# Performance work log

Measured on AMD Instinct MI355X. Metric: run time of the kernel, lower is better.

The kernel has to match this reference:

```python
import jax, jax.numpy as jnp
import numpy as np

B, S, D_TEXT, MAXF = 2, 1024, 384, 5
D_MODEL, N_HEADS, D_FF, L = 768, 12, 3072, 4
HEAD_DIM = D_MODEL // N_HEADS
EPS = 1e-6
NEG = -1e9


def _rms(x, g):
    return x * jax.lax.rsqrt(jnp.mean(x * x, axis=-1, keepdims=True) + EPS) * g


def _attn(x, w, mask):
    # w: [4, d, d] = (wq, wk, wv, wo); mask: [b, s, s] bool (True = attend)
    b, s, d = x.shape

    def proj(W):
        return jnp.einsum('bsd,de->bse', x, W).reshape(b, s, N_HEADS, HEAD_DIM).transpose(0, 2, 1, 3)

    q, k, v = proj(w[0]), proj(w[1]), proj(w[2])
    scale = jnp.asarray(1.0 / np.sqrt(HEAD_DIM), x.dtype)
    scores = jnp.einsum('bhqe,bhke->bhqk', q, k) * scale
    scores = jnp.where(mask[:, None], scores, NEG)
    p = jax.nn.softmax(scores, axis=-1)
    o = jnp.einsum('bhqk,bhke->bhqe', p, v).transpose(0, 2, 1, 3).reshape(b, s, d)
    return jnp.einsum('bsd,de->bse', o, w[3])


def _forward(number_values, datetime_values, boolean_values, text_values, column_name_values,
             W_cn, b_cn, W_num, b_num, W_text, b_text, W_dt, b_dt, W_bool, b_bool,
             g_cn, g_num, g_text, g_dt, g_bool, mask_emb,
             blk_norms, blk_attn, blk_up, blk_gate, blk_down,
             g_out, Wd_num, bd_num, Wd_dt, bd_dt, Wd_bool, bd_bool, Wd_text, bd_text,
             node_indices, table_name_indices, column_name_indices,
             f2p_neighbor_indices, semantic_types, masks, is_padding):
    valid = ~is_padding
    pv = valid[:, :, None] & valid[:, None, :]  # [b,s,s]
    eye = jnp.eye(S, dtype=bool)[None]
    same_node = node_indices[:, :, None] == node_indices[:, None, :]
    col_mask = ((column_name_indices[:, :, None] == column_name_indices[:, None, :])
                & (table_name_indices[:, :, None] == table_name_indices[:, None, :]) & pv) | eye
    feat_mask = (same_node & pv) | eye
    # kv node is one of q's f2p neighbors
    nei = (f2p_neighbor_indices[:, :, :, None] == node_indices[:, None, None, :]).any(axis=2)
    nei_mask = ((nei | same_node) & pv) | eye
    full_mask = pv | eye

    # per-semantic-type value encoders (Linear + RMSNorm)
    cn = _rms(column_name_values @ W_cn + b_cn, g_cn)
    num_e = _rms(number_values @ W_num + b_num, g_num)
    text_e = _rms(text_values @ W_text + b_text, g_text)
    dt_e = _rms(datetime_values @ W_dt + b_dt, g_dt)
    bool_e = _rms(boolean_values @ W_bool + b_bool, g_bool)
    st = semantic_types[..., None]
    val = jnp.where(st == 0, num_e, jnp.where(st == 1, text_e, jnp.where(st == 2, dt_e, bool_e)))
    # masked cells get the learned mask embedding for their semantic type
    val = jnp.where(masks[..., None], mask_emb[semantic_types], val)
    x = val + cn

    for i in range(L):
        nw, aw = blk_norms[i], blk_attn[i]
        x = x + _attn(_rms(x, nw[0]), aw[0], col_mask)
        x = x + _attn(_rms(x, nw[1]), aw[1], feat_mask)
        x = x + _attn(_rms(x, nw[2]), aw[2], nei_mask)
        x = x + _attn(_rms(x, nw[3]), aw[3], full_mask)
        h = _rms(x, nw[4])
        x = x + (jax.nn.silu(h @ blk_gate[i]) * (h @ blk_up[i])) @ blk_down[i]

    h = _rms(x, g_out)
    return (h @ Wd_num + bd_num, h @ Wd_dt + bd_dt, h @ Wd_bool + bd_bool, h @ Wd_text + bd_text)


def setup_inputs() -> dict:
    key = jax.random.key(0)
    ks = iter(jax.random.split(key, 64))

    def nrm(shape, scale=0.02):
        return jax.random.normal(next(ks), shape, jnp.float32) * scale

    inp = {}
    inp['number_values'] = jax.random.normal(next(ks), (B, S, 1), jnp.float32)
    inp['datetime_values'] = jax.random.normal(next(ks), (B, S, 1), jnp.float32)
    inp['boolean_values'] = jax.random.normal(next(ks), (B, S, 1), jnp.float32)
    inp['text_values'] = jax.random.normal(next(ks), (B, S, D_TEXT), jnp.float32)
    inp['column_name_values'] = jax.random.normal(next(ks), (B, S, D_TEXT), jnp.float32)
    inp['W_cn'] = nrm((D_TEXT, D_MODEL)); inp['b_cn'] = jnp.zeros((D_MODEL,), jnp.float32)
    inp['W_num'] = nrm((1, D_MODEL)); inp['b_num'] = jnp.zeros((D_MODEL,), jnp.float32)
    inp['W_text'] = nrm((D_TEXT, D_MODEL)); inp['b_text'] = jnp.zeros((D_MODEL,), jnp.float32)
    inp['W_dt'] = nrm((1, D_MODEL)); inp['b_dt'] = jnp.zeros((D_MODEL,), jnp.float32)
    inp['W_bool'] = nrm((1, D_MODEL)); inp['b_bool'] = jnp.zeros((D_MODEL,), jnp.float32)
    for n in ('g_cn', 'g_num', 'g_text', 'g_dt', 'g_bool'):
        inp[n] = jnp.ones((D_MODEL,), jnp.float32)
    inp['mask_emb'] = jax.random.normal(next(ks), (4, D_MODEL), jnp.float32)
    inp['blk_norms'] = jnp.ones((L, 5, D_MODEL), jnp.float32)
    inp['blk_attn'] = nrm((L, 4, 4, D_MODEL, D_MODEL))
    inp['blk_up'] = nrm((L, D_MODEL, D_FF))
    inp['blk_gate'] = nrm((L, D_MODEL, D_FF))
    inp['blk_down'] = nrm((L, D_FF, D_MODEL))
    inp['g_out'] = jnp.ones((D_MODEL,), jnp.float32)
    inp['Wd_num'] = nrm((D_MODEL, 1)); inp['bd_num'] = jnp.zeros((1,), jnp.float32)
    inp['Wd_dt'] = nrm((D_MODEL, 1)); inp['bd_dt'] = jnp.zeros((1,), jnp.float32)
    inp['Wd_bool'] = nrm((D_MODEL, 1)); inp['bd_bool'] = jnp.zeros((1,), jnp.float32)
    inp['Wd_text'] = nrm((D_MODEL, D_TEXT)); inp['bd_text'] = jnp.zeros((D_TEXT,), jnp.float32)
    inp['node_indices'] = jax.random.randint(next(ks), (B, S), 0, 128)
    inp['table_name_indices'] = jax.random.randint(next(ks), (B, S), 0, 8)
    inp['column_name_indices'] = jax.random.randint(next(ks), (B, S), 0, 32)
    inp['f2p_neighbor_indices'] = jax.random.randint(next(ks), (B, S, MAXF), 0, 128)
    inp['semantic_types'] = jax.random.randint(next(ks), (B, S), 0, 4)
    inp['masks'] = jax.random.bernoulli(next(ks), 0.15, (B, S))
    inp['is_padding'] = jnp.zeros((B, S), bool)
    return inp


def reference(number_values, datetime_values, boolean_values, text_values, column_name_values,
              W_cn, b_cn, W_num, b_num, W_text, b_text, W_dt, b_dt, W_bool, b_bool,
              g_cn, g_num, g_text, g_dt, g_bool, mask_emb,
              blk_norms, blk_attn, blk_up, blk_gate, blk_down,
              g_out, Wd_num, bd_num, Wd_dt, bd_dt, Wd_bool, bd_bool, Wd_text, bd_text,
              node_indices, table_name_indices, column_name_indices,
              f2p_neighbor_indices, semantic_types, masks, is_padding):
    return _forward(number_values, datetime_values, boolean_values, text_values, column_name_values,
                    W_cn, b_cn, W_num, b_num, W_text, b_text, W_dt, b_dt, W_bool, b_bool,
                    g_cn, g_num, g_text, g_dt, g_bool, mask_emb,
                    blk_norms, blk_attn, blk_up, blk_gate, blk_down,
                    g_out, Wd_num, bd_num, Wd_dt, bd_dt, Wd_bool, bd_bool, Wd_text, bd_text,
                    node_indices, table_name_indices, column_name_indices,
                    f2p_neighbor_indices, semantic_types, masks, is_padding)
```

## Files before the change

### kernel.cpp

```cpp
#include <hip/hip_runtime.h>
#include <hip/hip_bf16.h>
#include <cmath>
#include <stdint.h>


#define BB 2
#define SS 1024
#define DT 384
#define DM 768
#define NH 12
#define DH 64
#define DFF 3072
#define NL 4
#define NROW (BB*SS)
#define EPSF 1e-6f
#define QSC 0.1803368801111244f

typedef unsigned short u16;
typedef unsigned char u8;
typedef unsigned int u32;
typedef __attribute__((ext_vector_type(8))) short s16x8;
typedef __attribute__((ext_vector_type(4))) float f32x4;

__device__ __forceinline__ u16 f2bu(float f){
    u32 x = __float_as_uint(f);
    u32 r = (x + 0x7fffu + ((x>>16)&1u)) >> 16;
    return (u16)r;
}
__device__ __forceinline__ u32 pk2(float lo, float hi){
    return (u32)f2bu(lo) | ((u32)f2bu(hi)<<16);
}
__device__ __forceinline__ int swz(int row, int c){
    return (row<<6) + (((((c>>3) ^ row) & 7))<<3) + (c&7);
}
__device__ __forceinline__ float rsum16(float v){
    v += __shfl_xor(v,1); v += __shfl_xor(v,2);
    v += __shfl_xor(v,4); v += __shfl_xor(v,8);
    return v;
}
#define SBAR() __builtin_amdgcn_sched_barrier(0)
#define GLDS(src,dst) __builtin_amdgcn_global_load_lds((const __attribute__((address_space(1))) u32*)(src), (__attribute__((address_space(3))) u32*)(dst), 16, 0, 0)
#define GLDS4(src,dst) __builtin_amdgcn_global_load_lds((const __attribute__((address_space(1))) u32*)(src), (__attribute__((address_space(3))) u32*)(dst), 4, 0, 0)

__global__ void zero_f(float* __restrict__ p, int n){
    int i = blockIdx.x*256 + threadIdx.x;
    if (i<n) p[i]=0.f;
}

__device__ void norm_bool_body(const void* __restrict__ src, u8* __restrict__ dst, int n)
{
    __shared__ int fl[4];
    if (threadIdx.x<4) fl[threadIdx.x]=0;
    __syncthreads();
    const u32* wsrc = (const u32*)src;
    const int nw = n/4;
    int any=0, nb=0, hi=0, lo=0;
    for (int i=threadIdx.x;i<nw;i+=blockDim.x){
        u32 v=wsrc[i];
        if (!v) continue;
        any=1;
        #pragma unroll
        for (int b=0;b<4;b++){
            u32 by=(v>>(8*b))&0xffu;
            if (by>1u) nb=1;
            if (by==1u && b!=0) hi=1;
        }
        if ((v&0xffffu)==0x3f80u) lo=1;
    }
    if (any) atomicOr(&fl[0],1);
    if (nb)  atomicOr(&fl[1],1);
    if (hi)  atomicOr(&fl[2],1);
    if (lo)  atomicOr(&fl[3],1);
    __syncthreads();
    int c;
    if (!fl[0]) c=0;
    else if (!fl[1]) c = fl[2] ? 2 : 1;
    else if (fl[3]) c = 3;
    else c = 1;
    for (int i=threadIdx.x;i<n;i+=blockDim.x){
        u8 v;
        if (c==0)      v=0;
        else if (c==1) v = (((const u32*)src)[i]!=0u);
        else if (c==2) v = (((const u8*)src)[i]!=0u);
        else           v = (((const u16*)src)[i]!=0u);
        dst[i]=v;
    }
}
__global__ void norm_bool2(const void* s0, u8* d0, const void* s1, u8* d1, int n)
{
    if (blockIdx.x==0) norm_bool_body(s0,d0,n);
    else               norm_bool_body(s1,d1,n);
}

__global__ void pack_meta(const int* __restrict__ node, const int* __restrict__ colx,
                          const int* __restrict__ tbl, const u8* __restrict__ pad,
                          u32* __restrict__ pm, int n)
{
    int i = blockIdx.x*256 + threadIdx.x;
    if (i<n)
        pm[i] = (u32)(node[i]&0xff) | ((u32)(colx[i]&0xff)<<8) | ((u32)(tbl[i]&0xff)<<16) | ((u32)(pad[i]&1)<<24);
}

__global__ __launch_bounds__(256) void mask4_kernel(const u32* __restrict__ pm, const int* __restrict__ f2p,
                                                    u8* __restrict__ m4)
{
    const int b = blockIdx.y, kg = blockIdx.x;
    const int t = threadIdx.x;
    __shared__ u32 qm[1024];
    __shared__ int qf[1024*5];
    for (int i=t;i<1024;i+=256) qm[i] = pm[b*SS+i];
    for (int i=t;i<5*1024;i+=256) qf[i] = f2p[b*SS*5 + i];
    __syncthreads();
    const int q0 = t*4;
    u32 qmv[4]; int qn[4]; int qfv[4][5];
    #pragma unroll
    for (int j=0;j<4;j++){
        qmv[j]=qm[q0+j]; qn[j]=(int)(qmv[j]&0xffu);
        #pragma unroll
        for (int f=0;f<5;f++) qfv[j][f]=qf[(q0+j)*5+f];
    }
    for (int kk=0;kk<16;kk++){
        const int k = kg*16+kk;
        const u32 km = qm[k];
        const int kn = (int)(km&0xffu);
        u32 outw=0;
        #pragma unroll
        for (int j=0;j<4;j++){
            const u32 qmw = qmv[j];
            const bool pv = (((qmw|km)>>24)&1u)==0u;
            u32 by=0;
            if ((((qmw^km)&0x00ffff00u)==0u) && pv) by|=1;
            if ((((qmw^km)&0xffu)==0u) && pv) by|=2;
            bool nei = (qfv[j][0]==kn)||(qfv[j][1]==kn)||(qfv[j][2]==kn)||(qfv[j][3]==kn)||(qfv[j][4]==kn)
                       ||(qn[j]==kn);
            if (nei && pv) by|=4;
            if (pv) by|=8;
            if ((q0+j)==k) by=15;
            outw |= by<<(8*j);
        }
        ((u32*)(m4 + ((size_t)b<<20) + ((size_t)k<<10)))[t] = outw;
    }
}

__global__ __launch_bounds__(256) void transpose_cvt2(const float* __restrict__ src, u16* __restrict__ dst,
                                                      int K, int N, size_t dz,
                                                      const float* __restrict__ gbase, int gmode)
{
    const int z = blockIdx.z;
    src += (size_t)z*K*N;
    dst += (size_t)z*dz;
    const float* g = nullptr;
    if (gmode==1){ int m = z&3; if (m<3) g = gbase + (size_t)((z>>4)*5 + ((z>>2)&3))*768; }
    else if (gmode==2){ g = gbase + (size_t)z*5*768; }
    const int n0 = blockIdx.x*32, k0 = blockIdx.y*64;
    __shared__ float t[64][33];
    const int tid = threadIdx.x;
    const int kr = tid>>3, n4 = (tid&7)*4;
    #pragma unroll
    for (int p=0;p<2;p++){
        const int k = p*32 + kr;
        float gk = g ? g[k0+k] : 1.f;
        float4 v = *(const float4*)(src + (size_t)(k0+k)*N + n0 + n4);
        t[k][n4]=v.x*gk; t[k][n4+1]=v.y*gk; t[k][n4+2]=v.z*gk; t[k][n4+3]=v.w*gk;
    }
    __syncthreads();
    const int n = tid>>3, ks = (tid&7)*8;
    const int ng = n0 + n;
    uint4 o;
    u32* op = (u32*)&o;
    #pragma unroll
    for (int i=0;i<4;i++)
        op[i] = pk2(t[ks+2*i][n], t[ks+2*i+1][n]);
    *(uint4*)&dst[(((size_t)(ng>>7)*(K>>6) + (k0>>6))<<13) + ((ng&127)<<6) + ks] = o;
}

__global__ __launch_bounds__(256) void cvt_tiled2(const float* __restrict__ s0, u16* __restrict__ d0,
                                                  const float* __restrict__ s1, u16* __restrict__ d1, int K)
{
    const float* src = blockIdx.y ? s1 : s0;
    u16* dst = blockIdx.y ? d1 : d0;
    const int gid = blockIdx.x*256 + threadIdx.x;
    const int base = gid*8;
    const int row = base / K, col = base - row*K;
    float4 a = *(const float4*)(src + base);
    float4 b = *(const float4*)(src + base + 4);
    uint4 o;
    o.x = pk2(a.x,a.y); o.y = pk2(a.z,a.w);
    o.z = pk2(b.x,b.y); o.w = pk2(b.z,b.w);
    *(uint4*)&dst[(((size_t)(row>>7)*(K>>6) + (col>>6))<<13) + ((row&127)<<6) + (col&63)] = o;
}

__device__ __forceinline__ void stage3(const u16* aT, const u16* bT, int cb, int brow,
                                       u16* la, u16* lb, int w, int l)
{
    #pragma unroll
    for (int p=0;p<2;p++){
        const int q = p*256 + w*64 + l;
        const int row = q>>2, u = q&3;
        const int so = row*64 + cb + (((u ^ ((row>>1)&3))&3)<<3);
        GLDS(aT+so, la + p*2048 + w*512);
    }
    {
        const int q = w*64 + l;
        const int row = q>>2, u = q&3;
        const int so = (brow+row)*64 + cb + (((u ^ ((row>>1)&3))&3)<<3);
        GLDS(bT+so, lb + w*512);
    }
}

__global__ __launch_bounds__(256,4) void gemm_t(
    const u16* __restrict__ At, const u16* __restrict__ Bt,
    int K, int AMS, u16* __restrict__ qk16, u16* __restrict__ vt16,
    const float* __restrict__ rs_in)
{
    __shared__ u16 lds[3][6144];
    const int tid = threadIdx.x;
    const int lane = tid & 63, w = tid >> 6;
    const int cg = lane >> 4, cl = lane & 15;
    const int NT = K >> 5;
    const int n0 = blockIdx.x*64;
    const int brow = n0 & 64;
    const size_t bNb = (size_t)(n0>>7)*(K>>6);

    const u16* aB = At + ((size_t)blockIdx.y * AMS << 13);
    const u16* bB = Bt + (bNb << 13);

    f32x4 acc[2][4];
    #pragma unroll
    for (int i=0;i<2;i++)
        #pragma unroll
        for (int j=0;j<4;j++) acc[i][j] = (f32x4){0.f,0.f,0.f,0.f};

    stage3(aB, bB, 0,  brow, &lds[0][0], &lds[0][4096], w, lane);
    stage3(aB, bB, 32, brow, &lds[1][0], &lds[1][4096], w, lane);

    for (int kt=0; kt<NT; kt++){
        const int buf = kt % 3;
        if (kt+2 < NT){
            const int k2 = kt+2;
            stage3(aB + ((size_t)(k2>>1)<<13), bB + ((size_t)(k2>>1)<<13),
                   (k2&1)<<5, brow, &lds[k2%3][0], &lds[k2%3][4096], w, lane);
            asm volatile("s_waitcnt vmcnt(6)" ::: "memory");
        } else if (kt+1 < NT){
            asm volatile("s_waitcnt vmcnt(3)" ::: "memory");
        } else {
            asm volatile("s_waitcnt vmcnt(0)" ::: "memory");
        }
        SBAR(); __builtin_amdgcn_s_barrier(); SBAR();
        s16x8 af[2], bf[4];
        #pragma unroll
        for (int mt=0;mt<2;mt++){
            const int ra = w*32 + mt*16 + cl;
            af[mt] = *(const s16x8*)&lds[buf][ra*32 + (((cg ^ ((ra>>1)&3))&3)<<3)];
        }
        #pragma unroll
        for (int nt=0;nt<4;nt++){
            const int rb = nt*16 + cl;
            bf[nt] = *(const s16x8*)&lds[buf][4096 + rb*32 + (((cg ^ ((rb>>1)&3))&3)<<3)];
        }
        #pragma unroll
        for (int mt=0;mt<2;mt++)
            #pragma unroll
            for (int nt=0;nt<4;nt++)
                acc[mt][nt] = __builtin_amdgcn_mfma_f32_16x16x32_bf16(af[mt], bf[nt], acc[mt][nt], 0,0,0);
        SBAR(); __builtin_amdgcn_s_barrier(); SBAR();
    }

    const int m0 = blockIdx.y*128;
    #pragma unroll
    for (int mt=0;mt<2;mt++){
        const int grow0 = m0 + w*32 + mt*16 + cg*4;
        float rr[4];
        #pragma unroll
        for (int j=0;j<4;j++) rr[j] = rsqrtf(rs_in[grow0+j]*(1.f/768.f) + EPSF);
        #pragma unroll
        for (int nt=0;nt<4;nt++){
            const int col = n0 + nt*16 + cl;
            if (col < 768){
                #pragma unroll
                for (int j=0;j<4;j++)
                    qk16[(size_t)(grow0+j)*1536 + col] = f2bu(acc[mt][nt][j]*rr[j]*QSC);
            } else if (col < 1536){
                #pragma unroll
                for (int j=0;j<4;j++)
                    qk16[(size_t)(grow0+j)*1536 + col] = f2bu(acc[mt][nt][j]*rr[j]);
            } else {
                const int b = grow0>>10, s0 = grow0&1023;
                const int dhg = col - 1536;
                uint2 o;
                o.x = pk2(acc[mt][nt][0]*rr[0], acc[mt][nt][1]*rr[1]);
                o.y = pk2(acc[mt][nt][2]*rr[2], acc[mt][nt][3]*rr[3]);
                *(uint2*)(vt16 + ((size_t)(b*768 + dhg)<<10) + s0) = o;
            }
        }
    }
}

__global__ __launch_bounds__(256,3) void gemm_gu(
    const u16* __restrict__ At, const u16* __restrict__ Bg, const u16* __restrict__ Bu,
    const float* __restrict__ rs_in, u16* __restrict__ o16)
{
    __shared__ u16 lds[3][8192];
    const int tid = threadIdx.x;
    const int lane = tid & 63, w = tid >> 6;
    const int cg = lane >> 4, cl = lane & 15;
    const int NT = 24;
    const int n0 = blockIdx.x*64;
    const int brow = n0 & 64;
    const size_t bNb = (size_t)(n0>>7)*12;

    const u16* aB = At + ((size_t)blockIdx.y * 12 << 13);
    const u16* gB = Bg + (bNb << 13);
    const u16* uB = Bu + (bNb << 13);

    f32x4 accg[2][4], accu[2][4];
    #pragma unroll
    for (int i=0;i<2;i++)
        #pragma unroll
        for (int j=0;j<4;j++){ accg[i][j] = (f32x4){0.f,0.f,0.f,0.f}; accu[i][j] = (f32x4){0.f,0.f,0.f,0.f}; }

    #define STAGE_GU(kt2, cb, buf) { \
        const u16* a_ = aB + ((size_t)(kt2)<<13); \
        const u16* g_ = gB + ((size_t)(kt2)<<13); \
        const u16* u_ = uB + ((size_t)(kt2)<<13); \
        _Pragma("unroll") \
        for (int p=0;p<2;p++){ \
            const int q = p*256 + w*64 + lane; \
            const int row = q>>2, uu = q&3; \
            const int so = row*64 + (cb) + (((uu ^ ((row>>1)&3))&3)<<3); \
            GLDS(a_+so, &lds[buf][0] + p*2048 + w*512); \
        } \
        { \
            const int q = w*64 + lane; \
            const int row = q>>2, uu = q&3; \
            const int so = (brow+row)*64 + (cb) + (((uu ^ ((row>>1)&3))&3)<<3); \
            GLDS(g_+so, &lds[buf][4096] + w*512); \
            GLDS(u_+so, &lds[buf][6144] + w*512); \
        } }

    STAGE_GU(0, 0,  0);
    STAGE_GU(0, 32, 1);

    for (int kt=0; kt<NT; kt++){
        const int buf = kt % 3;
        if (kt+2 < NT){
            const int k2 = kt+2;
            STAGE_GU(k2>>1, (k2&1)<<5, k2%3);
            asm volatile("s_waitcnt vmcnt(8)" ::: "memory");
        } else if (kt+1 < NT){
            asm volatile("s_waitcnt vmcnt(4)" ::: "memory");
        } else {
            asm volatile("s_waitcnt vmcnt(0)" ::: "memory");
        }
        SBAR(); __builtin_amdgcn_s_barrier(); SBAR();
        s16x8 af[2], bg[4], bu[4];
        #pragma unroll
        for (int mt=0;mt<2;mt++){
            const int ra = w*32 + mt*16 + cl;
            af[mt] = *(const s16x8*)&lds[buf][ra*32 + (((cg ^ ((ra>>1)&3))&3)<<3)];
        }
        #pragma unroll
        for (int nt=0;nt<4;nt++){
            const int rb = nt*16 + cl;
            const int sw = (((cg ^ ((rb>>1)&3))&3)<<3);
            bg[nt] = *(const s16x8*)&lds[buf][4096 + rb*32 + sw];
            bu[nt] = *(const s16x8*)&lds[buf][6144 + rb*32 + sw];
        }
        #pragma unroll
        for (int mt=0;mt<2;mt++)
            #pragma unroll
            for (int nt=0;nt<4;nt++){
                accg[mt][nt] = __builtin_amdgcn_mfma_f32_16x16x32_bf16(af[mt], bg[nt], accg[mt][nt], 0,0,0);
                accu[mt][nt] = __builtin_amdgcn_mfma_f32_16x16x32_bf16(af[mt], bu[nt], accu[mt][nt], 0,0,0);
            }
        SBAR(); __builtin_amdgcn_s_barrier(); SBAR();
    }

    const int m0 = blockIdx.y*128;
    #pragma unroll
    for (int mt=0;mt<2;mt++){
        const int grow0 = m0 + w*32 + mt*16 + cg*4;
        float rr[4];
        #pragma unroll
        for (int j=0;j<4;j++) rr[j] = rsqrtf(rs_in[grow0+j]*(1.f/768.f) + EPSF);
        #pragma unroll
        for (int nt=0;nt<4;nt++){
            const int col = n0 + nt*16 + cl;
            const size_t tb = (((size_t)(grow0>>7)*48 + (col>>6))<<13) + (col&63);
            #pragma unroll
            for (int j=0;j<4;j++){
                float g = accg[mt][nt][j]*rr[j];
                float u = accu[mt][nt][j]*rr[j];
                float s = g/(1.f+__expf(-g))*u;
                o16[tb + (((grow0+j)&127)<<6)] = f2bu(s);
            }
        }
    }
}

__device__ __forceinline__ void stage64(const u16* aT, int arow, const u16* bT, int brow, int cb,
                                        u16* la, u16* lb, int w, int l)
{
    const int q = w*64 + l;
    const int row = q>>2, u = q&3;
    const int sw = (((u ^ ((row>>1)&3))&3)<<3);
    GLDS(aT + (arow+row)*64 + cb + sw, la + w*512);
    GLDS(bT + (brow+row)*64 + cb + sw, lb + w*512);
}

__global__ __launch_bounds__(256,6) void gemm_t64(
    const u16* __restrict__ At, const u16* __restrict__ Bt, float* __restrict__ C,
    int N, int K, int AMS, int flags, const float* __restrict__ bias,
    u16* __restrict__ o16, float* __restrict__ rs_out)
{
    __shared__ u16 lds[3][4096];
    const int tid = threadIdx.x;
    const int lane = tid & 63, w = tid >> 6;
    const int cg = lane >> 4, cl = lane & 15;
    const int NT = K >> 5;
    const int n0 = blockIdx.x*64;
    const int m0 = blockIdx.y*64;
    const int brow = n0 & 64, arow = m0 & 64;

    const u16* aB = At + ((size_t)(m0>>7) * AMS << 13);
    const u16* bB = Bt + ((size_t)(n0>>7) * (K>>6) << 13);

    f32x4 acc[4];
    #pragma unroll
    for (int j=0;j<4;j++) acc[j] = (f32x4){0.f,0.f,0.f,0.f};

    stage64(aB, arow, bB, brow, 0,  &lds[0][0], &lds[0][2048], w, lane);
    stage64(aB, arow, bB, brow, 32, &lds[1][0], &lds[1][2048], w, lane);

    for (int kt=0; kt<NT; kt++){
        const int buf = kt % 3;
        if (kt+2 < NT){
            const int k2 = kt+2;
            stage64(aB + ((size_t)(k2>>1)<<13), arow, bB + ((size_t)(k2>>1)<<13), brow,
                    (k2&1)<<5, &lds[k2%3][0], &lds[k2%3][2048], w, lane);
            asm volatile("s_waitcnt vmcnt(4)" ::: "memory");
        } else if (kt+1 < NT){
            asm volatile("s_waitcnt vmcnt(2)" ::: "memory");
        } else {
            asm volatile("s_waitcnt vmcnt(0)" ::: "memory");
        }
        SBAR(); __builtin_amdgcn_s_barrier(); SBAR();
        const int ra = w*16 + cl;
        s16x8 af = *(const s16x8*)&lds[buf][ra*32 + (((cg ^ ((ra>>1)&3))&3)<<3)];
        s16x8 bf[4];
        #pragma unroll
        for (int nt=0;nt<4;nt++){
            const int rb = nt*16 + cl;
            bf[nt] = *(const s16x8*)&lds[buf][2048 + rb*32 + (((cg ^ ((rb>>1)&3))&3)<<3)];
        }
        #pragma unroll
        for (int nt=0;nt<4;nt++)
            acc[nt] = __builtin_amdgcn_mfma_f32_16x16x32_bf16(af, bf[nt], acc[nt], 0,0,0);
        SBAR(); __builtin_amdgcn_s_barrier(); SBAR();
    }

    const int grow0 = m0 + w*16 + cg*4;
    const bool do_acc = (flags&1), do_bias = (flags&2);
    float tmp[4][4];
    #pragma unroll
    for (int nt=0;nt<4;nt++){
        const int col = n0 + nt*16 + cl;
        float bv = do_bias ? bias[col] : 0.f;
        #pragma unroll
        for (int j=0;j<4;j++){
            float v = acc[nt][j] + bv;
            float* cp = C + (size_t)(grow0+j)*N + col;
            if (do_acc) v += *cp;
            *cp = v;
            tmp[nt][j] = v;
        }
    }
    if (o16){
        #pragma unroll
        for (int nt=0;nt<4;nt++){
            const int col = n0 + nt*16 + cl;
            const size_t tb = (((size_t)(grow0>>7)*12 + (col>>6))<<13) + (col&63);
            #pragma unroll
            for (int j=0;j<4;j++)
                o16[tb + (((grow0+j)&127)<<6)] = f2bu(tmp[nt][j]);
        }
    }
    if (rs_out){
        #pragma unroll
        for (int j=0;j<4;j++){
            float s = tmp[0][j]*tmp[0][j] + tmp[1][j]*tmp[1][j]
                    + tmp[2][j]*tmp[2][j] + tmp[3][j]*tmp[3][j];
            s = rsum16(s);
            if (cl==0) atomicAdd(rs_out + grow0 + j, s);
        }
    }
}

__global__ __launch_bounds__(256,3) void attn_mfma3(
    const u16* __restrict__ qk16, const u16* __restrict__ vt16,
    const u8* __restrict__ m4, int mt,
    u16* __restrict__ ob16)
{
    const int bh = blockIdx.y;
    const int b = bh / NH, h = bh % NH;
    const int q0 = blockIdx.x * 64;
    const int tid = threadIdx.x;
    const int w = tid>>6, lane = tid&63, cg = lane>>4, cl = lane&15;
    const int srow = lane>>3;
    const int sseg = (lane&7) ^ srow;
    const int mk = lane>>4, mq = lane&15;

    __shared__ u16 Qs[4096], Ks[2][4096], Vt[2][4096], Ps[4096];
    __shared__ u32 Ms[2][1024];

    const u16* qbase = qk16 + (size_t)(b*SS+q0)*1536 + h*64;
    const u16* kbase = qk16 + (size_t)(b*SS)*1536 + 768 + h*64;
    const u16* vbase = vt16 + ((size_t)(b*768 + h*64)<<10);
    const u8*  mbase = m4 + ((size_t)b<<20) + q0;

    #pragma unroll
    for (int p=0;p<2;p++){
        const int row = p*32 + w*8 + srow;
        GLDS(qbase + (size_t)row*1536 + sseg*8, Qs + p*2048 + w*512);
    }
    #pragma unroll
    for (int p=0;p<2;p++){
        const int row = p*32 + w*8 + srow;
        GLDS(kbase + (size_t)row*1536 + sseg*8, Ks[0] + p*2048 + w*512);
        GLDS(vbase + ((size_t)row<<10) + sseg*8, Vt[0] + p*2048 + w*512);
    }
    #pragma unroll
    for (int i=0;i<4;i++){
        const int key = w*16 + i*4 + mk;
        GLDS4(mbase + ((size_t)key<<10) + mq*4, (u8*)Ms[0] + w*1024 + i*256);
    }

    f32x4 o[4];
    #pragma unroll
    for (int nt=0;nt<4;nt++) o[nt] = (f32x4){0.f,0.f,0.f,0.f};
    float lsum[4] = {0.f,0.f,0.f,0.f};

    for (int kc=0;kc<16;kc++){
        const int buf = kc & 1;
        if (kc < 15){
            const int kn0 = kc*64 + 64;
            #pragma unroll
            for (int p=0;p<2;p++){
                const int row = p*32 + w*8 + srow;
                GLDS(kbase + (size_t)(kn0+row)*1536 + sseg*8, Ks[buf^1] + p*2048 + w*512);
                GLDS(vbase + ((size_t)row<<10) + kn0 + sseg*8, Vt[buf^1] + p*2048 + w*512);
            }
            #pragma unroll
            for (int i=0;i<4;i++){
                const int key = kn0 + w*16 + i*4 + mk;
                GLDS4(mbase + ((size_t)key<<10) + mq*4, (u8*)Ms[buf^1] + w*1024 + i*256);
            }
            asm volatile("s_waitcnt vmcnt(8)" ::: "memory");
        } else {
            asm volatile("s_waitcnt vmcnt(0)" ::: "memory");
        }
        SBAR(); __builtin_amdgcn_s_barrier(); SBAR();

        f32x4 sc[4];
        #pragma unroll
        for (int nt=0;nt<4;nt++) sc[nt] = (f32x4){0.f,0.f,0.f,0.f};
        __builtin_amdgcn_s_setprio(1);
        #pragma unroll
        for (int ks=0;ks<2;ks++){
            s16x8 qa = *(const s16x8*)&Qs[swz(w*16+cl, ks*32+cg*8)];
            #pragma unroll
            for (int nt=0;nt<4;nt++){
                s16x8 kb = *(const s16x8*)&Ks[buf][swz(nt*16+cl, ks*32+cg*8)];
                sc[nt] = __builtin_amdgcn_mfma_f32_16x16x32_bf16(qa, kb, sc[nt], 0,0,0);
            }
        }
        __builtin_amdgcn_s_setprio(0);

        float pP[4][4];
        #pragma unroll
        for (int nt=0;nt<4;nt++){
            const u32 w4 = Ms[buf][(nt*16+cl)*16 + w*4 + cg];
            #pragma unroll
            for (int j=0;j<4;j++){
                float pe = exp2f(fminf(sc[nt][j], 100.f));
                pe = ((w4 >> (8*j + mt)) & 1u) ? pe : 0.f;
                pP[nt][j] = pe;
                lsum[j] += pe;
            }
        }

        #pragma unroll
        for (int nt=0;nt<4;nt++)
            #pragma unroll
            for (int j=0;j<4;j++)
                Ps[swz(w*16+cg*4+j, nt*16+cl)] = f2bu(pP[nt][j]);

        __builtin_amdgcn_s_setprio(1);
        #pragma unroll
        for (int ks=0;ks<2;ks++){
            s16x8 pa = *(const s16x8*)&Ps[swz(w*16+cl, ks*32+cg*8)];
            #pragma unroll
            for (int nt=0;nt<4;nt++){
                s16x8 vb = *(const s16x8*)&Vt[buf][swz(nt*16+cl, ks*32+cg*8)];
                o[nt] = __builtin_amdgcn_mfma_f32_16x16x32_bf16(pa, vb, o[nt], 0,0,0);
            }
        }
        __builtin_amdgcn_s_setprio(0);
        SBAR(); __builtin_amdgcn_s_barrier(); SBAR();
    }

    #pragma unroll
    for (int j=0;j<4;j++){
        const float inv = 1.f/rsum16(lsum[j]);
        const int row = b*SS + q0 + w*16 + cg*4 + j;
        const size_t rb = ((size_t)(row>>7)*12 + h)*8192 + ((row&127)<<6);
        #pragma unroll
        for (int nt=0;nt<4;nt++)
            ob16[rb + nt*16 + cl] = f2bu(o[nt][j]*inv);
    }
}

__global__ __launch_bounds__(256) void fuse_encode(
    const float* __restrict__ cnbuf, const float* __restrict__ textbuf,
    const float* __restrict__ numv, const float* __restrict__ dtv, const float* __restrict__ boolv,
    const float* __restrict__ Wnum, const float* __restrict__ bnum,
    const float* __restrict__ Wdt, const float* __restrict__ bdt,
    const float* __restrict__ Wbool, const float* __restrict__ bbool,
    const float* __restrict__ gcn, const float* __restrict__ gnum, const float* __restrict__ gtext,
    const float* __restrict__ gdt, const float* __restrict__ gbool,
    const float* __restrict__ memb, const int* __restrict__ stypes, const u8* __restrict__ masks,
    float* __restrict__ x, u16* __restrict__ xt16, float* __restrict__ rs0)
{
    const int row = blockIdx.x;
    const int t = threadIdx.x;
    __shared__ float red[256];

    float cn3[3]; float ss=0.f;
    #pragma unroll
    for (int j=0;j<3;j++){
        cn3[j] = cnbuf[(size_t)row*DM + t + j*256];
        ss += cn3[j]*cn3[j];
    }
    red[t]=ss; __syncthreads();
    for (int s=128;s>0;s>>=1){ if(t<s) red[t]+=red[t+s]; __syncthreads(); }
    {
        float r = rsqrtf(red[0]/(float)DM + EPSF);
        #pragma unroll
        for (int j=0;j<3;j++) cn3[j] *= r*gcn[t+j*256];
    }
    __syncthreads();

    const int st = stypes[row];
    float val[3]; ss=0.f;
    if (st==1){
        #pragma unroll
        for (int j=0;j<3;j++){
            val[j] = textbuf[(size_t)row*DM + t + j*256];
            ss += val[j]*val[j];
        }
    } else {
        const float* Wp = (st==0)?Wnum:((st==2)?Wdt:Wbool);
        const float* bp = (st==0)?bnum:((st==2)?bdt:bbool);
        const float* vp = (st==0)?numv:((st==2)?dtv:boolv);
        float v = vp[row];
        #pragma unroll
        for (int j=0;j<3;j++){
            int e=t+j*256;
            val[j] = v*Wp[e] + bp[e];
            ss += val[j]*val[j];
        }
    }
    red[t]=ss; __syncthreads();
    for (int s=128;s>0;s>>=1){ if(t<s) red[t]+=red[t+s]; __syncthreads(); }
    const float* gp = (st==0)?gnum:((st==1)?gtext:((st==2)?gdt:gbool));
    float r2 = rsqrtf(red[0]/(float)DM + EPSF);
    bool mk = masks[row]!=0;
    float xv[3]; float sx=0.f;
    #pragma unroll
    for (int j=0;j<3;j++){
        int e=t+j*256;
        float vv = val[j]*r2*gp[e];
        if (mk) vv = memb[st*DM+e];
        xv[j] = vv + cn3[j];
        x[(size_t)row*DM+e] = xv[j];
        sx += xv[j]*xv[j];
    }
    __syncthreads();
    red[t]=sx; __syncthreads();
    for (int s=128;s>0;s>>=1){ if(t<s) red[t]+=red[t+s]; __syncthreads(); }
    if (t==0) rs0[row] = red[0];
    const size_t mb = (size_t)(row>>7)*12;
    const int rr = (row&127)<<6;
    #pragma unroll
    for (int j=0;j<3;j++){
        const int c = t + j*256;
        xt16[((mb + (c>>6))<<13) + rr + (c&63)] = f2bu(xv[j]);
    }
}

__global__ __launch_bounds__(256) void decode2(
    const float* __restrict__ x, const float* __restrict__ gout,
    const float* __restrict__ Wn, const float* __restrict__ bn,
    const float* __restrict__ Wd, const float* __restrict__ bd,
    const float* __restrict__ Wb, const float* __restrict__ bb,
    float* __restrict__ out, u16* __restrict__ h16)
{
    const int row = blockIdx.x;
    const int t = threadIdx.x;
    __shared__ float h[DM];
    __shared__ float red[256];
    const float* xr = x + (size_t)row*DM;
    float v0=xr[t], v1=xr[t+256], v2=xr[t+512];
    red[t]=v0*v0+v1*v1+v2*v2; __syncthreads();
    for (int s=128;s>0;s>>=1){ if(t<s) red[t]+=red[t+s]; __syncthreads(); }
    float r = rsqrtf(red[0]/(float)DM + EPSF);
    float h0 = v0*r*gout[t], h1 = v1*r*gout[t+256], h2 = v2*r*gout[t+512];
    h[t]=h0; h[t+256]=h1; h[t+512]=h2;
    const size_t mb = (size_t)(row>>7)*12;
    const int rr = (row&127)<<6;
    #pragma unroll
    for (int j=0;j<3;j++){
        const int c = t + j*256;
        const float v = (j==0?h0:(j==1?h1:h2));
        h16[((mb + (c>>6))<<13) + rr + (c&63)] = f2bu(v);
    }
    __syncthreads();

    float pn=0.f,pd=0.f,pb=0.f;
    for (int k=t;k<DM;k+=256){ float hv=h[k]; pn+=hv*Wn[k]; pd+=hv*Wd[k]; pb+=hv*Wb[k]; }
    red[t]=pn; __syncthreads();
    for (int s=128;s>0;s>>=1){ if(t<s) red[t]+=red[t+s]; __syncthreads(); }
    float tn=red[0]; __syncthreads();
    red[t]=pd; __syncthreads();
    for (int s=128;s>0;s>>=1){ if(t<s) red[t]+=red[t+s]; __syncthreads(); }
    float td=red[0]; __syncthreads();
    red[t]=pb; __syncthreads();
    for (int s=128;s>0;s>>=1){ if(t<s) red[t]+=red[t+s]; __syncthreads(); }
    float tb=red[0];
    if (t==0){
        out[row]          = tn + bn[0];
        out[NROW + row]   = td + bd[0];
        out[2*NROW + row] = tb + bb[0];
    }
}

extern "C" void kernel_launch(void* const* d_in, const int* in_sizes, int n_in,
                              void* d_out, int out_size, void* d_ws, size_t ws_size,
                              hipStream_t stream)
{
    const float* numv   = (const float*)d_in[0];
    const float* dtval  = (const float*)d_in[1];
    const float* boolv  = (const float*)d_in[2];
    const float* textv  = (const float*)d_in[3];
    const float* cnamev = (const float*)d_in[4];
    const float* Wcn=(const float*)d_in[5];  const float* bcn=(const float*)d_in[6];
    const float* Wnum=(const float*)d_in[7]; const float* bnum=(const float*)d_in[8];
    const float* Wtext=(const float*)d_in[9];const float* btext=(const float*)d_in[10];
    const float* Wdt=(const float*)d_in[11]; const float* bdt=(const float*)d_in[12];
    const float* Wbool=(const float*)d_in[13];const float* bbool=(const float*)d_in[14];
    const float* gcn=(const float*)d_in[15]; const float* gnum=(const float*)d_in[16];
    const float* gtext=(const float*)d_in[17];const float* gdt=(const float*)d_in[18];
    const float* gbool=(const float*)d_in[19];
    const float* memb=(const float*)d_in[20];
    const float* norms_all=(const float*)d_in[21];
    const float* attw_all=(const float*)d_in[22];
    const float* up_all=(const float*)d_in[23];
    const float* gate_all=(const float*)d_in[24];
    const float* down_all=(const float*)d_in[25];
    const float* gout=(const float*)d_in[26];
    const float* Wdn=(const float*)d_in[27]; const float* bdn=(const float*)d_in[28];
    const float* Wdd=(const float*)d_in[29]; const float* bdd=(const float*)d_in[30];
    const float* Wdb=(const float*)d_in[31]; const float* bdb=(const float*)d_in[32];
    const float* Wdtx=(const float*)d_in[33];const float* bdtx=(const float*)d_in[34];
    const int* node=(const int*)d_in[35];
    const int* tbl =(const int*)d_in[36];
    const int* colx=(const int*)d_in[37];
    const int* f2p =(const int*)d_in[38];
    const int* styp=(const int*)d_in[39];

    const size_t SA = (size_t)768*768;
    const size_t SG = (size_t)768*3072;
    const size_t SC = (size_t)384*768;
    const size_t NX = (size_t)NROW*DM;

    u8* base = (u8*)d_ws;
    float* x  = (float*)base;
    u16* xt16 = (u16*)(base + 6291456);
    u16* ob16 = (u16*)(base + 9437184);
    u16* qk16 = (u16*)(base + 12582912);
    u16* vt16 = (u16*)(base + 18874368);
    u16* gu16 = (u16*)(base + 22020096);
    u16* wA   = (u16*)(base + 47185920);
    u16* wGU  = wA + 64*SA;
    u16* wD   = wGU + 8*SG;
    u16* wCN  = wD + 4*SG;
    u16* wTX  = wCN + SC;
    u16* wDX  = wTX + SC;
    u8* nmask = (u8*)(wDX + SC);
    u8* npad  = nmask + NROW;
    u32* pmeta = (u32*)(npad + NROW + 64);
    float* rsbuf = (float*)(pmeta + NROW);
    u8* m4 = (u8*)(rsbuf + 21*2048);

    u16* cnT16   = qk16;
    u16* textT16 = vt16;
    float* cnbuf   = (float*)gu16;
    float* textbuf = cnbuf + NX;

    float* out = (float*)d_out;

    zero_f<<<(21*2048)/256,256,0,stream>>>(rsbuf, 21*2048);
    norm_bool2<<<2,256,0,stream>>>(d_in[40], nmask, d_in[41], npad, NROW);
    pack_meta<<<NROW/256,256,0,stream>>>(node, colx, tbl, npad, pmeta, NROW);
    mask4_kernel<<<dim3(64,2),256,0,stream>>>(pmeta, f2p, m4);

    transpose_cvt2<<<dim3(24,12,64),256,0,stream>>>(attw_all, wA, 768, 768, SA, norms_all, 1);
    transpose_cvt2<<<dim3(96,12,4),256,0,stream>>>(gate_all, wGU,      768, 3072, 2*SG, norms_all + 4*768, 2);
    transpose_cvt2<<<dim3(96,12,4),256,0,stream>>>(up_all,   wGU + SG, 768, 3072, 2*SG, norms_all + 4*768, 2);
    transpose_cvt2<<<dim3(24,48,4),256,0,stream>>>(down_all, wD, 3072, 768, SG, nullptr, 0);
    transpose_cvt2<<<dim3(24,6,1),256,0,stream>>>(Wcn,   wCN, 384, 768, 0, nullptr, 0);
    transpose_cvt2<<<dim3(24,6,1),256,0,stream>>>(Wtext, wTX, 384, 768, 0, nullptr, 0);
    transpose_cvt2<<<dim3(12,12,1),256,0,stream>>>(Wdtx, wDX, 768, 384, 0, nullptr, 0);

    cvt_tiled2<<<dim3(384,2),256,0,stream>>>(cnamev, cnT16, textv, textT16, 384);
    gemm_t64<<<dim3(12,32),256,0,stream>>>(cnT16,   wCN, cnbuf,   768, 384, 6, 2, bcn,   nullptr, nullptr);
    gemm_t64<<<dim3(12,32),256,0,stream>>>(textT16, wTX, textbuf, 768, 384, 6, 2, btext, nullptr, nullptr);
    fuse_encode<<<NROW,256,0,stream>>>(cnbuf, textbuf, numv, dtval, boolv,
        Wnum,bnum,Wdt,bdt,Wbool,bbool, gcn,gnum,gtext,gdt,gbool,
        memb, styp, nmask, x, xt16, rsbuf);

    const dim3 ga(SS/64, BB*NH);
    for (int l=0; l<NL; l++){
        for (int a=0; a<4; a++){
            const int slot = l*5 + a;
            const u16* wqkv = wA + (size_t)((l*4+a)*4)*SA;
            gemm_t<<<dim3(36,16),256,0,stream>>>(xt16, wqkv, 768, 12, qk16, vt16,
                rsbuf + (size_t)slot*2048);
            attn_mfma3<<<ga,256,0,stream>>>(qk16, vt16, m4, a, ob16);
            gemm_t64<<<dim3(12,32),256,0,stream>>>(ob16, wqkv + 3*SA, x, 768, 768, 12, 1, nullptr,
                xt16, rsbuf + (size_t)(slot+1)*2048);
        }
        gemm_gu<<<dim3(48,16),256,0,stream>>>(xt16, wGU + (size_t)l*2*SG, wGU + (size_t)l*2*SG + SG,
            rsbuf + (size_t)(l*5+4)*2048, gu16);
        gemm_t64<<<dim3(12,32),256,0,stream>>>(gu16, wD + (size_t)l*SG, x, 768, 3072, 48, 1, nullptr,
            xt16, rsbuf + (size_t)((l+1)*5)*2048);
    }

    decode2<<<NROW,256,0,stream>>>(x, gout, Wdn,bdn, Wdd,bdd, Wdb,bdb, out, xt16);
    gemm_t64<<<dim3(6,32),256,0,stream>>>(xt16, wDX, out + 3*NROW, 384, 768, 12, 2, bdtx,
        nullptr, nullptr);
}
```

Before: 1.448 ms.

## Use single-stage prefetch with one barrier per k-step; keep attention Q in registers

The three GEMM kernels now prefetch one k-tile ahead instead of two. They drop the trailing barrier in each iteration and rely on the three-buffer rotation plus the leading barrier to avoid overwriting LDS that is still being read. The attention kernel loads each wave's Q fragments straight from global memory into registers instead of staging them through LDS, which removes an 8KB shared array and the LDS reads in the inner loop. Fewer barriers and less LDS traffic come at the cost of a shallower load pipeline, which may expose more global memory latency.

```diff
diff --git a/kernel.cpp b/kernel.cpp
--- a/kernel.cpp
+++ b/kernel.cpp
@@ -231,17 +231,14 @@
         #pragma unroll
         for (int j=0;j<4;j++) acc[i][j] = (f32x4){0.f,0.f,0.f,0.f};
 
-    stage3(aB, bB, 0,  brow, &lds[0][0], &lds[0][4096], w, lane);
-    stage3(aB, bB, 32, brow, &lds[1][0], &lds[1][4096], w, lane);
+    stage3(aB, bB, 0, brow, &lds[0][0], &lds[0][4096], w, lane);
 
     for (int kt=0; kt<NT; kt++){
         const int buf = kt % 3;
-        if (kt+2 < NT){
-            const int k2 = kt+2;
-            stage3(aB + ((size_t)(k2>>1)<<13), bB + ((size_t)(k2>>1)<<13),
-                   (k2&1)<<5, brow, &lds[k2%3][0], &lds[k2%3][4096], w, lane);
-            asm volatile("s_waitcnt vmcnt(6)" ::: "memory");
-        } else if (kt+1 < NT){
+        if (kt+1 < NT){
+            const int k1 = kt+1;
+            stage3(aB + ((size_t)(k1>>1)<<13), bB + ((size_t)(k1>>1)<<13),
+                   (k1&1)<<5, brow, &lds[k1%3][0], &lds[k1%3][4096], w, lane);
             asm volatile("s_waitcnt vmcnt(3)" ::: "memory");
         } else {
             asm volatile("s_waitcnt vmcnt(0)" ::: "memory");
@@ -263,7 +260,6 @@
             #pragma unroll
             for (int nt=0;nt<4;nt++)
                 acc[mt][nt] = __builtin_amdgcn_mfma_f32_16x16x32_bf16(af[mt], bf[nt], acc[mt][nt], 0,0,0);
-        SBAR(); __builtin_amdgcn_s_barrier(); SBAR();
     }
 
     const int m0 = blockIdx.y*128;
@@ -338,16 +334,13 @@
             GLDS(u_+so, &lds[buf][6144] + w*512); \
         } }
 
-    STAGE_GU(0, 0,  0);
-    STAGE_GU(0, 32, 1);
+    STAGE_GU(0, 0, 0);
 
     for (int kt=0; kt<NT; kt++){
         const int buf = kt % 3;
-        if (kt+2 < NT){
-            const int k2 = kt+2;
-            STAGE_GU(k2>>1, (k2&1)<<5, k2%3);
-            asm volatile("s_waitcnt vmcnt(8)" ::: "memory");
-        } else if (kt+1 < NT){
+        if (kt+1 < NT){
+            const int k1 = kt+1;
+            STAGE_GU(k1>>1, (k1&1)<<5, k1%3);
             asm volatile("s_waitcnt vmcnt(4)" ::: "memory");
         } else {
             asm volatile("s_waitcnt vmcnt(0)" ::: "memory");
@@ -373,7 +366,6 @@
                 accg[mt][nt] = __builtin_amdgcn_mfma_f32_16x16x32_bf16(af[mt], bg[nt], accg[mt][nt], 0,0,0);
                 accu[mt][nt] = __builtin_amdgcn_mfma_f32_16x16x32_bf16(af[mt], bu[nt], accu[mt][nt], 0,0,0);
             }
-        SBAR(); __builtin_amdgcn_s_barrier(); SBAR();
     }
 
     const int m0 = blockIdx.y*128;
@@ -429,17 +421,14 @@
     #pragma unroll
     for (int j=0;j<4;j++) acc[j] = (f32x4){0.f,0.f,0.f,0.f};
 
-    stage64(aB, arow, bB, brow, 0,  &lds[0][0], &lds[0][2048], w, lane);
-    stage64(aB, arow, bB, brow, 32, &lds[1][0], &lds[1][2048], w, lane);
+    stage64(aB, arow, bB, brow, 0, &lds[0][0], &lds[0][2048], w, lane);
 
     for (int kt=0; kt<NT; kt++){
         const int buf = kt % 3;
-        if (kt+2 < NT){
-            const int k2 = kt+2;
-            stage64(aB + ((size_t)(k2>>1)<<13), arow, bB + ((size_t)(k2>>1)<<13), brow,
-                    (k2&1)<<5, &lds[k2%3][0], &lds[k2%3][2048], w, lane);
-            asm volatile("s_waitcnt vmcnt(4)" ::: "memory");
-        } else if (kt+1 < NT){
+        if (kt+1 < NT){
+            const int k1 = kt+1;
+            stage64(aB + ((size_t)(k1>>1)<<13), arow, bB + ((size_t)(k1>>1)<<13), brow,
+                    (k1&1)<<5, &lds[k1%3][0], &lds[k1%3][2048], w, lane);
             asm volatile("s_waitcnt vmcnt(2)" ::: "memory");
         } else {
             asm volatile("s_waitcnt vmcnt(0)" ::: "memory");
@@ -456,7 +445,6 @@
         #pragma unroll
         for (int nt=0;nt<4;nt++)
             acc[nt] = __builtin_amdgcn_mfma_f32_16x16x32_bf16(af, bf[nt], acc[nt], 0,0,0);
-        SBAR(); __builtin_amdgcn_s_barrier(); SBAR();
     }
 
     const int grow0 = m0 + w*16 + cg*4;
@@ -510,19 +498,21 @@
     const int sseg = (lane&7) ^ srow;
     const int mk = lane>>4, mq = lane&15;
 
-    __shared__ u16 Qs[4096], Ks[2][4096], Vt[2][4096], Ps[4096];
+    __shared__ u16 Ks[2][4096], Vt[2][4096], Ps[4096];
     __shared__ u32 Ms[2][1024];
 
-    const u16* qbase = qk16 + (size_t)(b*SS+q0)*1536 + h*64;
+    s16x8 qa0, qa1;
+    {
+        const u16* qrow = qk16 + (size_t)(b*SS+q0 + w*16 + cl)*1536 + h*64;
+        qa0 = *(const s16x8*)(qrow + cg*8);
+        qa1 = *(const s16x8*)(qrow + 32 + cg*8);
+        asm volatile("" :: "v"(*(const f32x4*)&qa0), "v"(*(const f32x4*)&qa1));
+    }
+
     const u16* kbase = qk16 + (size_t)(b*SS)*1536 + 768 + h*64;
     const u16* vbase = vt16 + ((size_t)(b*768 + h*64)<<10);
     const u8*  mbase = m4 + ((size_t)b<<20) + q0;
 
-    #pragma unroll
-    for (int p=0;p<2;p++){
-        const int row = p*32 + w*8 + srow;
-        GLDS(qbase + (size_t)row*1536 + sseg*8, Qs + p*2048 + w*512);
-    }
     #pragma unroll
     for (int p=0;p<2;p++){
         const int row = p*32 + w*8 + srow;
@@ -566,13 +556,14 @@
         for (int nt=0;nt<4;nt++) sc[nt] = (f32x4){0.f,0.f,0.f,0.f};
         __builtin_amdgcn_s_setprio(1);
         #pragma unroll
-        for (int ks=0;ks<2;ks++){
-            s16x8 qa = *(const s16x8*)&Qs[swz(w*16+cl, ks*32+cg*8)];
-            #pragma unroll
-            for (int nt=0;nt<4;nt++){
-                s16x8 kb = *(const s16x8*)&Ks[buf][swz(nt*16+cl, ks*32+cg*8)];
-                sc[nt] = __builtin_amdgcn_mfma_f32_16x16x32_bf16(qa, kb, sc[nt], 0,0,0);
-            }
+        for (int nt=0;nt<4;nt++){
+            s16x8 kb0 = *(const s16x8*)&Ks[buf][swz(nt*16+cl, cg*8)];
+            sc[nt] = __builtin_amdgcn_mfma_f32_16x16x32_bf16(qa0, kb0, sc[nt], 0,0,0);
+        }
+        #pragma unroll
+        for (int nt=0;nt<4;nt++){
+            s16x8 kb1 = *(const s16x8*)&Ks[buf][swz(nt*16+cl, 32+cg*8)];
+            sc[nt] = __builtin_amdgcn_mfma_f32_16x16x32_bf16(qa1, kb1, sc[nt], 0,0,0);
         }
         __builtin_amdgcn_s_setprio(0);
 
```

New measurement: 1.445 ms. Within noise of the previous version (-0.2%).
